# Kernel optimization log

Measured on AMD Instinct MI355X. Metric: run time of the kernel, lower is better.

Reference implementation:

```python
import jax, jax.numpy as jnp
import numpy as np

S, B, H = 2048, 2, 4096
NH, NG, HD = 32, 8, 128  # heads, kv groups, head size


def setup_inputs() -> dict:
    key = jax.random.key(0)
    k1, k2, k3 = jax.random.split(key, 3)
    x = jax.random.normal(k1, (S, B, H), jnp.float32)
    qkv_h = H + 2 * HD * NG  # 6144
    W_qkv = jax.random.normal(k2, (qkv_h, H), jnp.float32) * 0.02
    b_qkv = jnp.zeros((qkv_h,), jnp.float32)
    W_dense = jax.random.normal(k3, (H, H), jnp.float32) * 0.02
    # rope cache: gen_rope_cache(S, n_elem=HD) -> [S, HD//2, 2] (cos, sin)
    theta = 1.0 / (10000.0 ** (jnp.arange(0, HD, 2, dtype=jnp.float32) / HD))
    ang = jnp.outer(jnp.arange(S, dtype=jnp.float32), theta)
    rope_cache = jnp.stack([jnp.cos(ang), jnp.sin(ang)], axis=-1)
    return {"x": x, "rope_cache": rope_cache, "W_qkv": W_qkv, "b_qkv": b_qkv, "W_dense": W_dense}


def _apply_rope(x, rope):
    # x: [S, B, nh, D]; rope: [S, D//2, 2]
    s, b, nh, d = x.shape
    half = rope.shape[1]
    rot = 2 * half
    xr = x[..., :rot].reshape(s, b, nh, half, 2)
    cos = rope[:s, None, None, :, 0]
    sin = rope[:s, None, None, :, 1]
    out = jnp.stack([xr[..., 0] * cos - xr[..., 1] * sin,
                     xr[..., 1] * cos + xr[..., 0] * sin], axis=-1)
    return jnp.concatenate([out.reshape(s, b, nh, rot), x[..., rot:]], axis=-1)


def reference(x, rope_cache, W_qkv, b_qkv, W_dense):
    s, b, h = x.shape
    qkv = x @ W_qkv.T + b_qkv  # [S, B, H + 2*NG*HD]
    q, k, v = jnp.split(qkv, [h, h + NG * HD], axis=-1)
    q = q.reshape(s, b, NH, HD)
    k = k.reshape(s, b, NG, HD)
    v = v.reshape(s, b, NG, HD)
    q = _apply_rope(q, rope_cache)
    k = _apply_rope(k, rope_cache)
    rep = NH // NG  # GQA expand: each kv group repeated contiguously (expand+view)
    k = jnp.repeat(k, rep, axis=2)
    v = jnp.repeat(v, rep, axis=2)
    q, k, v = (t.transpose(1, 2, 0, 3) for t in (q, k, v))  # [B, NH, S, HD]
    scale = 1.0 / jnp.sqrt(jnp.asarray(HD, x.dtype))
    scores = jnp.einsum('bhqd,bhkd->bhqk', q, k) * scale
    causal = jnp.tril(jnp.ones((s, s), bool))
    scores = jnp.where(causal, scores, jnp.finfo(scores.dtype).min)
    attn = jax.nn.softmax(scores, axis=-1)
    out = jnp.einsum('bhqk,bhkd->bhqd', attn, v)
    out = out.transpose(2, 0, 1, 3).reshape(s, b, h)  # [S, B, H]
    return out @ W_dense.T
```

## Files before the change

### kernel.cpp

```cpp
#include <hip/hip_runtime.h>
#include <hip/hip_bf16.h>
#include <cstdint>
#include <cstddef>

#define S_LEN   2048
#define BATCH   2
#define HDIM    4096
#define NHEADS  32
#define NGROUPS 8
#define HEADD   128
#define QKV_N   6144

typedef __attribute__((ext_vector_type(8))) short  short8;
typedef __attribute__((ext_vector_type(4))) float  floatx4;

__device__ __forceinline__ void async_ld16(const void* g, void* l) {
  __builtin_amdgcn_global_load_lds((const __attribute__((address_space(1))) void*)g,
                                   (__attribute__((address_space(3))) void*)l,
                                   16, 0, 0);
}

__device__ __forceinline__ unsigned short f2bf_bits(float f) {
  unsigned int u = __float_as_uint(f);
  u += 0x7FFFu + ((u >> 16) & 1u);
  return (unsigned short)(u >> 16);
}

__global__ void cvt_f32_bf16(const float4* __restrict__ in,
                             ushort4* __restrict__ out, int n4)
{
  const int i = blockIdx.x * blockDim.x + threadIdx.x;
  if (i >= n4) return;
  const float4 v = in[i];
  ushort4 o;
  o.x = f2bf_bits(v.x); o.y = f2bf_bits(v.y);
  o.z = f2bf_bits(v.z); o.w = f2bf_bits(v.w);
  out[i] = o;
}

template<int MODE>
__global__ void gemm128(const __hip_bfloat16* __restrict__ A,
                        const __hip_bfloat16* __restrict__ Bm,
                        const float* __restrict__ bias,
                        float* __restrict__ Cout,
                        __hip_bfloat16* __restrict__ Qbuf,
                        __hip_bfloat16* __restrict__ Kbuf,
                        __hip_bfloat16* __restrict__ Vtbuf,
                        int M, int N, int K)
{
  __shared__ short As[128*64];
  __shared__ short Bs[128*64];
  const int mb = blockIdx.y, nb = blockIdx.x;
  const int tid  = threadIdx.x;
  const int wave = tid >> 6, lane = tid & 63;
  const int wm = wave >> 1, wn = wave & 1;
  const int quad = lane >> 4, l15 = lane & 15;

  floatx4 acc[4][4] = {};

  const __hip_bfloat16* Abase = A  + (size_t)mb * 128 * K;
  const __hip_bfloat16* Bbase = Bm + (size_t)nb * 128 * K;

  for (int kb = 0; kb < K; kb += 64) {
    #pragma unroll
    for (int i = 0; i < 4; ++i) {
      const int cb  = (i*4 + wave) * 64;
      const int idx = cb + lane;
      const int r   = idx >> 3, cl = idx & 7;
      const int gc  = cl ^ (r & 7);
      async_ld16(Abase + (size_t)r*K + kb + gc*8, As + cb*8);
      async_ld16(Bbase + (size_t)r*K + kb + gc*8, Bs + cb*8);
    }
    __syncthreads();

    #pragma unroll
    for (int ks = 0; ks < 2; ++ks) {
      short8 af[4], bf[4];
      #pragma unroll
      for (int mi = 0; mi < 4; ++mi) {
        const int row = wm*64 + mi*16 + l15;
        const int ch  = (ks*4 + quad) ^ (l15 & 7);
        af[mi] = *(const short8*)&As[row*64 + ch*8];
      }
      #pragma unroll
      for (int ni = 0; ni < 4; ++ni) {
        const int row = wn*64 + ni*16 + l15;
        const int ch  = (ks*4 + quad) ^ (l15 & 7);
        bf[ni] = *(const short8*)&Bs[row*64 + ch*8];
      }
      #pragma unroll
      for (int mi = 0; mi < 4; ++mi)
        #pragma unroll
        for (int ni = 0; ni < 4; ++ni)
          acc[mi][ni] = __builtin_amdgcn_mfma_f32_16x16x32_bf16(
              af[mi], bf[ni], acc[mi][ni], 0, 0, 0);
    }
    __syncthreads();
  }

  #pragma unroll
  for (int mi = 0; mi < 4; ++mi) {
    #pragma unroll
    for (int ni = 0; ni < 4; ++ni) {
      const int n = nb*128 + wn*64 + ni*16 + l15;
      float bv = 0.0f;
      if (MODE == 1) bv = bias[n];
      #pragma unroll
      for (int r = 0; r < 4; ++r) {
        const int m = mb*128 + wm*64 + mi*16 + quad*4 + r;
        const float v = acc[mi][ni][r] + bv;
        if (MODE == 0) {
          Cout[(size_t)m*N + n] = v;
        } else {
          const __hip_bfloat16 hv = __float2bfloat16(v);
          const int s  = m >> 1;
          const int bi = m & 1;
          if (n < HDIM) {
            const int hh = n >> 7, d = n & 127;
            Qbuf[(((size_t)bi*NHEADS + hh)*S_LEN + s)*HEADD + d] = hv;
          } else if (n < HDIM + NGROUPS*HEADD) {
            const int gg = (n - HDIM) >> 7, d = n & 127;
            Kbuf[(((size_t)bi*NGROUPS + gg)*S_LEN + s)*HEADD + d] = hv;
          } else {
            const int gg = (n - (HDIM + NGROUPS*HEADD)) >> 7, d = n & 127;
            Vtbuf[(((size_t)bi*NGROUPS + gg)*HEADD + d)*S_LEN + s] = hv;
          }
        }
      }
    }
  }
}

__global__ void rope_kernel(__hip_bfloat16* __restrict__ Qbuf,
                            __hip_bfloat16* __restrict__ Kbuf,
                            const float* __restrict__ rope)
{
  const int QP = BATCH*NHEADS*S_LEN*64;
  const int KP = BATCH*NGROUPS*S_LEN*64;
  int idx = blockIdx.x * blockDim.x + threadIdx.x;
  __hip_bfloat16* base;
  int p;
  float post;
  if (idx < QP)            { base = Qbuf; p = idx;      post = 0.12751744061558475f; }
  else if (idx < QP + KP)  { base = Kbuf; p = idx - QP; post = 1.0f; }
  else return;
  const int i    = p & 63;
  const int rest = p >> 6;
  const int s    = rest & (S_LEN - 1);
  const float c  = rope[s*128 + 2*i];
  const float sn = rope[s*128 + 2*i + 1];
  __hip_bfloat16* ptr = base + (size_t)rest*HEADD + 2*i;
  const float x0 = __bfloat162float(ptr[0]);
  const float x1 = __bfloat162float(ptr[1]);
  ptr[0] = __float2bfloat16((x0*c - x1*sn) * post);
  ptr[1] = __float2bfloat16((x1*c + x0*sn) * post);
}

__global__ void __launch_bounds__(256)
attn_kernel(const __hip_bfloat16* __restrict__ Qbuf,
            const __hip_bfloat16* __restrict__ Kbuf,
            const __hip_bfloat16* __restrict__ Vtbuf,
            __hip_bfloat16* __restrict__ Obuf)
{
  __shared__ __align__(16) short KtS[64*128];
  __shared__ __align__(16) short VtS[128*64];
  __shared__ __align__(16) short PtS[4][16*72];

  const int qb   = blockIdx.x * 64;
  const int bh   = blockIdx.y;
  const int b    = bh >> 5, h = bh & 31;
  const int g    = h >> 2;
  const int tid  = threadIdx.x;
  const int wave = tid >> 6, lane = tid & 63;
  const int quad = lane >> 4, l15 = lane & 15;
  const int qw   = qb + wave*16;

  const __hip_bfloat16* Qp = Qbuf  + ((size_t)bh*S_LEN + qw) * HEADD;
  const __hip_bfloat16* Kp = Kbuf  + ((size_t)(b*NGROUPS + g)*S_LEN) * HEADD;
  const __hip_bfloat16* Vp = Vtbuf + ((size_t)(b*NGROUPS + g)*HEADD) * S_LEN;

  short8 aq[4];
  #pragma unroll
  for (int dc = 0; dc < 4; ++dc)
    aq[dc] = *(const short8*)&Qp[(size_t)l15*HEADD + dc*32 + quad*8];

  floatx4 O[8] = {};
  float li[4] = {0.f, 0.f, 0.f, 0.f};

  const int ktend = qb + 64;
  for (int kt = 0; kt < ktend; kt += 64) {
    #pragma unroll
    for (int i = 0; i < 4; ++i) {
      const int cb  = (i*4 + wave) * 64;
      const int idx = cb + lane;
      {
        const int r = idx >> 4, cl = idx & 15;
        const int gc = cl ^ (r & 15);
        async_ld16(Kp + (size_t)(kt + r)*HEADD + gc*8, KtS + cb*8);
      }
      {
        const int r = idx >> 3, cl = idx & 7;
        const int gc = cl ^ (r & 7);
        async_ld16(Vp + (size_t)r*S_LEN + kt + gc*8, VtS + cb*8);
      }
    }
    __syncthreads();

    floatx4 s[4] = {};
    #pragma unroll
    for (int dc = 0; dc < 4; ++dc) {
      #pragma unroll
      for (int kc = 0; kc < 4; ++kc) {
        const int row = kc*16 + l15;
        const int ch  = (dc*4 + quad) ^ l15;
        const short8 bk = *(const short8*)&KtS[row*128 + ch*8];
        s[kc] = __builtin_amdgcn_mfma_f32_16x16x32_bf16(aq[dc], bk, s[kc], 0, 0, 0);
      }
    }

    if (kt == qb) {
      #pragma unroll
      for (int r = 0; r < 4; ++r) {
        const int row = qw + quad*4 + r;
        float rs = 0.f;
        #pragma unroll
        for (int kc = 0; kc < 4; ++kc) {
          const int col = kt + kc*16 + l15;
          const float p = (col > row) ? 0.0f : __builtin_amdgcn_exp2f(s[kc][r]);
          s[kc][r] = p; rs += p;
        }
        li[r] += rs;
      }
    } else {
      #pragma unroll
      for (int r = 0; r < 4; ++r) {
        float rs = 0.f;
        #pragma unroll
        for (int kc = 0; kc < 4; ++kc) {
          const float p = __builtin_amdgcn_exp2f(s[kc][r]);
          s[kc][r] = p; rs += p;
        }
        li[r] += rs;
      }
    }

    #pragma unroll
    for (int r = 0; r < 4; ++r)
      #pragma unroll
      for (int kc = 0; kc < 4; ++kc)
        PtS[wave][(quad*4 + r)*72 + kc*16 + l15] = (short)f2bf_bits(s[kc][r]);
    const short8 pa0 = *(const short8*)&PtS[wave][l15*72 +      quad*8];
    const short8 pa1 = *(const short8*)&PtS[wave][l15*72 + 32 + quad*8];

    #pragma unroll
    for (int dt = 0; dt < 8; ++dt) {
      const int row = dt*16 + l15;
      const int c0 = quad ^ (l15 & 7);
      const int c1 = (4 + quad) ^ (l15 & 7);
      const short8 bv0 = *(const short8*)&VtS[row*64 + c0*8];
      const short8 bv1 = *(const short8*)&VtS[row*64 + c1*8];
      O[dt] = __builtin_amdgcn_mfma_f32_16x16x32_bf16(pa0, bv0, O[dt], 0, 0, 0);
      O[dt] = __builtin_amdgcn_mfma_f32_16x16x32_bf16(pa1, bv1, O[dt], 0, 0, 0);
    }
    __syncthreads();
  }

  float inv[4];
  #pragma unroll
  for (int r = 0; r < 4; ++r) {
    float l = li[r];
    l += __shfl_xor(l, 1, 16);
    l += __shfl_xor(l, 2, 16);
    l += __shfl_xor(l, 4, 16);
    l += __shfl_xor(l, 8, 16);
    inv[r] = 1.0f / l;
  }
  #pragma unroll
  for (int dt = 0; dt < 8; ++dt)
    #pragma unroll
    for (int r = 0; r < 4; ++r) {
      const int row = qw + quad*4 + r;
      Obuf[((size_t)row*BATCH + b)*HDIM + h*HEADD + dt*16 + l15] =
          __float2bfloat16(O[dt][r] * inv[r]);
    }
}

extern "C" void kernel_launch(void* const* d_in, const int* in_sizes, int n_in,
                              void* d_out, int out_size, void* d_ws, size_t ws_size,
                              hipStream_t stream)
{
  const float* x    = (const float*)d_in[0];
  const float* rope = (const float*)d_in[1];
  const float* Wqkv = (const float*)d_in[2];
  const float* bqkv = (const float*)d_in[3];
  const float* Wd   = (const float*)d_in[4];
  float* out = (float*)d_out;

  const size_t MiB = 1024*1024;
  char* ws = (char*)d_ws;
  __hip_bfloat16* xb    = (__hip_bfloat16*)(ws);
  __hip_bfloat16* Wqkvb = (__hip_bfloat16*)(ws + 32*MiB);
  __hip_bfloat16* Wdb   = (__hip_bfloat16*)(ws + 80*MiB);
  __hip_bfloat16* Qbuf  = (__hip_bfloat16*)(ws + 112*MiB);
  __hip_bfloat16* Kbuf  = (__hip_bfloat16*)(ws + 144*MiB);
  __hip_bfloat16* Vt    = (__hip_bfloat16*)(ws + 152*MiB);
  __hip_bfloat16* Ob    = (__hip_bfloat16*)(ws + 160*MiB);

  {
    const int nx = S_LEN*BATCH*HDIM/4;
    const int nq = QKV_N*HDIM/4;
    const int nd = HDIM*HDIM/4;
    cvt_f32_bf16<<<(nx+255)/256, 256, 0, stream>>>((const float4*)x,    (ushort4*)xb,    nx);
    cvt_f32_bf16<<<(nq+255)/256, 256, 0, stream>>>((const float4*)Wqkv, (ushort4*)Wqkvb, nq);
    cvt_f32_bf16<<<(nd+255)/256, 256, 0, stream>>>((const float4*)Wd,   (ushort4*)Wdb,   nd);
  }

  dim3 g1(QKV_N/128, (S_LEN*BATCH)/128);
  gemm128<1><<<g1, 256, 0, stream>>>(xb, Wqkvb, bqkv, nullptr,
                                     Qbuf, Kbuf, Vt,
                                     S_LEN*BATCH, QKV_N, HDIM);

  const int total_pairs = BATCH*(NHEADS+NGROUPS)*S_LEN*64;
  rope_kernel<<<total_pairs/256, 256, 0, stream>>>(Qbuf, Kbuf, rope);

  dim3 ga(S_LEN/64, BATCH*NHEADS);
  attn_kernel<<<ga, 256, 0, stream>>>(Qbuf, Kbuf, Vt, Ob);

  dim3 g2(HDIM/128, (S_LEN*BATCH)/128);
  gemm128<0><<<g2, 256, 0, stream>>>(Ob, Wdb, nullptr, out,
                                     nullptr, nullptr, nullptr,
                                     S_LEN*BATCH, HDIM, HDIM);
}
```

Baseline: 777.5 us.

## Read V directly from global in attention, merge conversions, add priorities

The attention kernel no longer stages V tiles in shared memory. Each wave loads its V fragments straight from global memory inside the PV loop, which frees LDS and lets launch_bounds ask for 4 blocks per CU. It also raises wave priority around the MFMA sections and folds the three fp32-to-bf16 conversion launches into one kernel. The cost is uncoalesced, unswizzled global reads of V on the critical path, with only L1/L2 to hide their latency.

Result: slower. 1.148 ms (+47.7%).

```diff
diff --git a/kernel.cpp b/kernel.cpp
--- a/kernel.cpp
+++ b/kernel.cpp
@@ -26,16 +26,25 @@
   return (unsigned short)(u >> 16);
 }
 
-__global__ void cvt_f32_bf16(const float4* __restrict__ in,
-                             ushort4* __restrict__ out, int n4)
-{
-  const int i = blockIdx.x * blockDim.x + threadIdx.x;
-  if (i >= n4) return;
-  const float4 v = in[i];
+__global__ void cvt_all(const float4* __restrict__ x,
+                        const float4* __restrict__ wq,
+                        const float4* __restrict__ wd,
+                        ushort4* __restrict__ xo,
+                        ushort4* __restrict__ wqo,
+                        ushort4* __restrict__ wdo,
+                        int nx, int nq, int nd)
+{
+  int i = blockIdx.x * blockDim.x + threadIdx.x;
+  const float4* src; ushort4* dst; int off;
+  if (i < nx)                { src = x;  dst = xo;  off = i; }
+  else if (i < nx + nq)      { src = wq; dst = wqo; off = i - nx; }
+  else if (i < nx + nq + nd) { src = wd; dst = wdo; off = i - nx - nq; }
+  else return;
+  const float4 v = src[off];
   ushort4 o;
   o.x = f2bf_bits(v.x); o.y = f2bf_bits(v.y);
   o.z = f2bf_bits(v.z); o.w = f2bf_bits(v.w);
-  out[i] = o;
+  dst[off] = o;
 }
 
 template<int MODE>
@@ -156,14 +165,13 @@
   ptr[1] = __float2bfloat16((x1*c + x0*sn) * post);
 }
 
-__global__ void __launch_bounds__(256)
+__global__ void __launch_bounds__(256, 4)
 attn_kernel(const __hip_bfloat16* __restrict__ Qbuf,
             const __hip_bfloat16* __restrict__ Kbuf,
             const __hip_bfloat16* __restrict__ Vtbuf,
             __hip_bfloat16* __restrict__ Obuf)
 {
   __shared__ __align__(16) short KtS[64*128];
-  __shared__ __align__(16) short VtS[128*64];
   __shared__ __align__(16) short PtS[4][16*72];
 
   const int qb   = blockIdx.x * 64;
@@ -193,20 +201,14 @@
     for (int i = 0; i < 4; ++i) {
       const int cb  = (i*4 + wave) * 64;
       const int idx = cb + lane;
-      {
-        const int r = idx >> 4, cl = idx & 15;
-        const int gc = cl ^ (r & 15);
-        async_ld16(Kp + (size_t)(kt + r)*HEADD + gc*8, KtS + cb*8);
-      }
-      {
-        const int r = idx >> 3, cl = idx & 7;
-        const int gc = cl ^ (r & 7);
-        async_ld16(Vp + (size_t)r*S_LEN + kt + gc*8, VtS + cb*8);
-      }
+      const int r = idx >> 4, cl = idx & 15;
+      const int gc = cl ^ (r & 15);
+      async_ld16(Kp + (size_t)(kt + r)*HEADD + gc*8, KtS + cb*8);
     }
     __syncthreads();
 
     floatx4 s[4] = {};
+    __builtin_amdgcn_s_setprio(1);
     #pragma unroll
     for (int dc = 0; dc < 4; ++dc) {
       #pragma unroll
@@ -217,6 +219,7 @@
         s[kc] = __builtin_amdgcn_mfma_f32_16x16x32_bf16(aq[dc], bk, s[kc], 0, 0, 0);
       }
     }
+    __builtin_amdgcn_s_setprio(0);
 
     if (kt == qb) {
       #pragma unroll
@@ -252,16 +255,17 @@
     const short8 pa0 = *(const short8*)&PtS[wave][l15*72 +      quad*8];
     const short8 pa1 = *(const short8*)&PtS[wave][l15*72 + 32 + quad*8];
 
+    __builtin_amdgcn_s_setprio(1);
     #pragma unroll
     for (int dt = 0; dt < 8; ++dt) {
       const int row = dt*16 + l15;
-      const int c0 = quad ^ (l15 & 7);
-      const int c1 = (4 + quad) ^ (l15 & 7);
-      const short8 bv0 = *(const short8*)&VtS[row*64 + c0*8];
-      const short8 bv1 = *(const short8*)&VtS[row*64 + c1*8];
+      const short8 bv0 = *(const short8*)&Vp[(size_t)row*S_LEN + kt      + quad*8];
+      const short8 bv1 = *(const short8*)&Vp[(size_t)row*S_LEN + kt + 32 + quad*8];
       O[dt] = __builtin_amdgcn_mfma_f32_16x16x32_bf16(pa0, bv0, O[dt], 0, 0, 0);
       O[dt] = __builtin_amdgcn_mfma_f32_16x16x32_bf16(pa1, bv1, O[dt], 0, 0, 0);
     }
+    __builtin_amdgcn_s_setprio(0);
+
     __syncthreads();
   }
 
@@ -310,9 +314,10 @@
     const int nx = S_LEN*BATCH*HDIM/4;
     const int nq = QKV_N*HDIM/4;
     const int nd = HDIM*HDIM/4;
-    cvt_f32_bf16<<<(nx+255)/256, 256, 0, stream>>>((const float4*)x,    (ushort4*)xb,    nx);
-    cvt_f32_bf16<<<(nq+255)/256, 256, 0, stream>>>((const float4*)Wqkv, (ushort4*)Wqkvb, nq);
-    cvt_f32_bf16<<<(nd+255)/256, 256, 0, stream>>>((const float4*)Wd,   (ushort4*)Wdb,   nd);
+    const int nt = nx + nq + nd;
+    cvt_all<<<(nt+255)/256, 256, 0, stream>>>(
+        (const float4*)x, (const float4*)Wqkv, (const float4*)Wd,
+        (ushort4*)xb, (ushort4*)Wqkvb, (ushort4*)Wdb, nx, nq, nd);
   }
 
   dim3 g1(QKV_N/128, (S_LEN*BATCH)/128);
```
